# Kernel optimization log

Hardware: AMD Instinct MI355X
Metric: run time of the kernel (lower is better)

Reference implementation:

```python
import jax, jax.numpy as jnp
import numpy as np

B, S, H = 64, 4096, 256

def setup_inputs() -> dict:
    key = jax.random.key(0)
    k1, k2, k3, k4, k5 = jax.random.split(key, 5)
    scale = 1.0 / np.sqrt(H)
    return {
        "enc_out": jax.random.normal(k1, (B, S, H), dtype=jnp.float32),
        "final_h": jax.random.normal(k2, (B, H), dtype=jnp.float32),
        "W1": jax.random.normal(k3, (H, H), dtype=jnp.float32) * scale,
        "W2": jax.random.normal(k4, (H, H), dtype=jnp.float32) * scale,
        "v": jax.random.normal(k5, (H,), dtype=jnp.float32) * scale,
    }

def reference(enc_out, final_h, W1, W2, v):
    # W1(enc_out): [B,S,H]; W2(final_h) computed once: [B,H], broadcast over S
    proj = jnp.einsum('bsh,kh->bsk', enc_out, W1) + jnp.einsum('bh,kh->bk', final_h, W2)[:, None, :]
    scores = jnp.einsum('bsk,k->bs', jnp.tanh(proj), v)  # [B,S]
    alpha = jax.nn.softmax(scores, axis=1)  # softmax over seq dim
    context = jnp.einsum('bs,bsh->bh', alpha, enc_out)  # [B,H]
    return context
```

## Files before the change

### kernel.cpp

```cpp
#include <hip/hip_runtime.h>

typedef _Float16 half8  __attribute__((ext_vector_type(8)));
typedef _Float16 half4_t __attribute__((ext_vector_type(4)));
typedef float    f32x4  __attribute__((ext_vector_type(4)));

#define B_SZ    64
#define S_SZ    4096
#define H_SZ    256
#define CHUNKS  8
#define SCHUNK  512
#define TILE_R  32
#define NTILES  (SCHUNK / TILE_R)
#define PAD_H   264

__device__ __forceinline__ float tanh_fast(float x) {
  return 1.f - 2.f * __builtin_amdgcn_rcpf(__expf(2.f * x) + 1.f);
}

__device__ __forceinline__ void lds_barrier() {
  asm volatile("s_waitcnt lgkmcnt(0)" ::: "memory");
  __builtin_amdgcn_s_barrier();
}

template<int CTRL>
__device__ __forceinline__ float dpp_add_shl(float x) {
  int s = __builtin_amdgcn_update_dpp(0, __builtin_bit_cast(int, x), CTRL, 0xf, 0xf, true);
  return x + __builtin_bit_cast(float, s);
}
__device__ __forceinline__ float row_reduce16(float x) {
  x = dpp_add_shl<0x108>(x);
  x = dpp_add_shl<0x104>(x);
  x = dpp_add_shl<0x102>(x);
  x = dpp_add_shl<0x101>(x);
  return x;
}

__global__ __launch_bounds__(256) void bias_kernel(const float* __restrict__ fh,
                                                   const float* __restrict__ W2,
                                                   float* __restrict__ bias) {
  const int b = blockIdx.x, k = threadIdx.x;
  __shared__ float fsh[H_SZ];
  fsh[k] = fh[b * H_SZ + k];
  __syncthreads();
  const float* wrow = W2 + (size_t)k * H_SZ;
  float s = 0.f;
#pragma unroll 4
  for (int h = 0; h < H_SZ; h += 4) {
    f32x4 w = *(const f32x4*)(wrow + h);
    s += w[0] * fsh[h] + w[1] * fsh[h + 1] + w[2] * fsh[h + 2] + w[3] * fsh[h + 3];
  }
  bias[b * H_SZ + k] = s;
}

__global__ __launch_bounds__(512, 2) void fused_kernel(const float* __restrict__ enc,
                                                       const float* __restrict__ W1,
                                                       const float* __restrict__ v,
                                                       const float* __restrict__ bias,
                                                       float* __restrict__ pc,
                                                       float* __restrict__ pl) {
  __shared__ _Float16 As[3][TILE_R][PAD_H] __attribute__((aligned(16)));
  __shared__ float spartT[2][TILE_R][12];
  __shared__ float cpart[8][H_SZ];
  __shared__ float lArr[8];

  const int tid  = threadIdx.x;
  const int wave = tid >> 6;
  const int lane = tid & 63;
  const int nlo  = lane & 15;
  const int g    = lane >> 4;
  const int khi  = g * 8;
  const int b     = blockIdx.x >> 3;
  const int chunk = blockIdx.x & 7;
  const size_t encBase = ((size_t)b * S_SZ + (size_t)chunk * SCHUNK) * H_SZ;
  const float* src0 = enc + encBase + (size_t)tid * 4;

  f32x4 ldA[4], ldB[4];
#pragma unroll
  for (int i = 0; i < 4; ++i) ldA[i] = *(const f32x4*)(src0 + i * 2048);

  half8 wf[2][8];
#pragma unroll
  for (int cf = 0; cf < 2; ++cf) {
    const int n = wave * 32 + cf * 16 + nlo;
    const float* wrow = W1 + (size_t)n * H_SZ + khi;
#pragma unroll
    for (int ks = 0; ks < 8; ++ks) {
      f32x4 w0 = *(const f32x4*)(wrow + ks * 32);
      f32x4 w1 = *(const f32x4*)(wrow + ks * 32 + 4);
      half8 h;
#pragma unroll
      for (int j = 0; j < 4; ++j) { h[j] = (_Float16)w0[j]; h[4 + j] = (_Float16)w1[j]; }
      wf[cf][ks] = h;
    }
  }
#pragma unroll
  for (int i = 0; i < 4; ++i) ldB[i] = *(const f32x4*)(src0 + TILE_R * H_SZ + i * 2048);

  const int n0c = wave * 32 + nlo;
  const float vv0 = v[n0c],               vv1 = v[n0c + 16];
  const float bv0 = bias[b * H_SZ + n0c], bv1 = bias[b * H_SZ + n0c + 16];

  float l_acc = 0.f;
  float c0 = 0.f, c1 = 0.f, c2 = 0.f, c3 = 0.f;

  int p = 0;
  int pm1 = 2;

  auto tile_iter = [&](int t, f32x4 (&ld)[4]) {
#pragma unroll
    for (int i = 0; i < 4; ++i) {
      const int f4 = tid + i * 512;
      const int r = f4 >> 6, hq = (f4 & 63) * 4;
      half4_t hv;
      hv[0] = (_Float16)ld[i][0]; hv[1] = (_Float16)ld[i][1];
      hv[2] = (_Float16)ld[i][2]; hv[3] = (_Float16)ld[i][3];
      *(half4_t*)&As[p][r][hq] = hv;
    }
    if (t + 2 < NTILES) {
      const float* srcN = src0 + (size_t)(t + 2) * TILE_R * H_SZ;
#pragma unroll
      for (int i = 0; i < 4; ++i) ld[i] = *(const f32x4*)(srcN + i * 2048);
    }
    lds_barrier();

#pragma unroll
    for (int rf = 0; rf < 2; ++rf) {
      f32x4 d0 = {bv0, bv0, bv0, bv0}, d1 = {bv1, bv1, bv1, bv1};
#pragma unroll
      for (int ks = 0; ks < 8; ++ks) {
        half8 a = *(const half8*)&As[p][rf * 16 + nlo][ks * 32 + khi];
        d0 = __builtin_amdgcn_mfma_f32_16x16x32_f16(a, wf[0][ks], d0, 0, 0, 0);
        d1 = __builtin_amdgcn_mfma_f32_16x16x32_f16(a, wf[1][ks], d1, 0, 0, 0);
      }
      f32x4 s4;
#pragma unroll
      for (int i = 0; i < 4; ++i)
        s4[i] = tanh_fast(d0[i]) * vv0 + tanh_fast(d1[i]) * vv1;
#pragma unroll
      for (int i = 0; i < 4; ++i) s4[i] = row_reduce16(s4[i]);
      if (nlo == 0) {
#pragma unroll
        for (int i = 0; i < 4; ++i) spartT[t & 1][rf * 16 + g * 4 + i][wave] = s4[i];
      }
    }

    if (t > 0) {
#pragma unroll
      for (int rr = 0; rr < 4; ++rr) {
        const int r = wave * 4 + rr;
        const f32x4 q0 = *(const f32x4*)&spartT[(t - 1) & 1][r][0];
        const f32x4 q1 = *(const f32x4*)&spartT[(t - 1) & 1][r][4];
        const float u = __expf(q0[0] + q0[1] + q0[2] + q0[3] + q1[0] + q1[1] + q1[2] + q1[3]);
        l_acc += u;
        half4_t a = *(const half4_t*)&As[pm1][r][lane * 4];
        c0 += u * (float)a[0];
        c1 += u * (float)a[1];
        c2 += u * (float)a[2];
        c3 += u * (float)a[3];
      }
    }
    pm1 = p;
    p = (p == 2) ? 0 : p + 1;
  };

#pragma unroll 1
  for (int t2 = 0; t2 < NTILES; t2 += 2) {
    tile_iter(t2,     ldA);
    tile_iter(t2 + 1, ldB);
  }

  lds_barrier();
  {
    const int tl = (NTILES - 1) & 1;
#pragma unroll
    for (int rr = 0; rr < 4; ++rr) {
      const int r = wave * 4 + rr;
      const f32x4 q0 = *(const f32x4*)&spartT[tl][r][0];
      const f32x4 q1 = *(const f32x4*)&spartT[tl][r][4];
      const float u = __expf(q0[0] + q0[1] + q0[2] + q0[3] + q1[0] + q1[1] + q1[2] + q1[3]);
      l_acc += u;
      half4_t a = *(const half4_t*)&As[pm1][r][lane * 4];
      c0 += u * (float)a[0];
      c1 += u * (float)a[1];
      c2 += u * (float)a[2];
      c3 += u * (float)a[3];
    }
  }

  {
    f32x4 cv; cv[0] = c0; cv[1] = c1; cv[2] = c2; cv[3] = c3;
    *(f32x4*)&cpart[wave][lane * 4] = cv;
  }
  if (lane == 0) lArr[wave] = l_acc;
  __syncthreads();
  if (tid < H_SZ) {
    float s = 0.f;
#pragma unroll
    for (int w = 0; w < 8; ++w) s += cpart[w][tid];
    pc[(size_t)blockIdx.x * H_SZ + tid] = s;
  }
  if (tid == 0) {
    float L = 0.f;
#pragma unroll
    for (int w = 0; w < 8; ++w) L += lArr[w];
    pl[blockIdx.x] = L;
  }
}

__global__ __launch_bounds__(256) void combine_kernel(const float* __restrict__ pc,
                                                      const float* __restrict__ pl,
                                                      float* __restrict__ out) {
  const int b = blockIdx.x, h = threadIdx.x;
  float L = 0.f, s = 0.f;
#pragma unroll
  for (int j = 0; j < CHUNKS; ++j) {
    L += pl[b * CHUNKS + j];
    s += pc[(size_t)(b * CHUNKS + j) * H_SZ + h];
  }
  out[b * H_SZ + h] = s / L;
}

extern "C" void kernel_launch(void* const* d_in, const int* in_sizes, int n_in,
                              void* d_out, int out_size, void* d_ws, size_t ws_size,
                              hipStream_t stream) {
  const float* enc = (const float*)d_in[0];
  const float* fh  = (const float*)d_in[1];
  const float* W1  = (const float*)d_in[2];
  const float* W2  = (const float*)d_in[3];
  const float* v   = (const float*)d_in[4];
  float* out = (float*)d_out;

  float* ws   = (float*)d_ws;
  float* bias = ws;
  float* pc   = ws + B_SZ * H_SZ;
  float* pl   = pc + B_SZ * CHUNKS * H_SZ;

  bias_kernel<<<B_SZ, H_SZ, 0, stream>>>(fh, W2, bias);
  fused_kernel<<<B_SZ * CHUNKS, 512, 0, stream>>>(enc, W1, v, bias, pc, pl);
  combine_kernel<<<B_SZ, H_SZ, 0, stream>>>(pc, pl, out);
}
```

Measured before the change: 86.67 us.

## Fuse combine into main kernel via last-block atomic counter, split prefetch loads

Removes the separate combine kernel launch. The last block of each batch to finish, detected with an atomic counter that the bias kernel resets, now reduces the chunk partials and writes the output. The global prefetch of the next tile is also split into two halves, each issued after one row-fragment's MFMA chain, to interleave loads with compute. This adds threadfences and an atomic per block, and the prefetch registers stay live in a different pattern.

Result: slower. 207.1 us (+138.9%).

```diff
diff --git a/kernel.cpp b/kernel.cpp
--- a/kernel.cpp
+++ b/kernel.cpp
@@ -37,8 +37,10 @@
 
 __global__ __launch_bounds__(256) void bias_kernel(const float* __restrict__ fh,
                                                    const float* __restrict__ W2,
-                                                   float* __restrict__ bias) {
+                                                   float* __restrict__ bias,
+                                                   int* __restrict__ cnt) {
   const int b = blockIdx.x, k = threadIdx.x;
+  if (k == 0) cnt[b] = 0;
   __shared__ float fsh[H_SZ];
   fsh[k] = fh[b * H_SZ + k];
   __syncthreads();
@@ -57,11 +59,14 @@
                                                        const float* __restrict__ v,
                                                        const float* __restrict__ bias,
                                                        float* __restrict__ pc,
-                                                       float* __restrict__ pl) {
+                                                       float* __restrict__ pl,
+                                                       int* __restrict__ cnt,
+                                                       float* __restrict__ out) {
   __shared__ _Float16 As[3][TILE_R][PAD_H] __attribute__((aligned(16)));
   __shared__ float spartT[2][TILE_R][12];
   __shared__ float cpart[8][H_SZ];
   __shared__ float lArr[8];
+  __shared__ int winner;
 
   const int tid  = threadIdx.x;
   const int wave = tid >> 6;
@@ -116,22 +121,23 @@
       hv[2] = (_Float16)ld[i][2]; hv[3] = (_Float16)ld[i][3];
       *(half4_t*)&As[p][r][hq] = hv;
     }
-    if (t + 2 < NTILES) {
-      const float* srcN = src0 + (size_t)(t + 2) * TILE_R * H_SZ;
-#pragma unroll
-      for (int i = 0; i < 4; ++i) ld[i] = *(const f32x4*)(srcN + i * 2048);
-    }
     lds_barrier();
 
-#pragma unroll
-    for (int rf = 0; rf < 2; ++rf) {
+    const bool pf = (t + 2 < NTILES);
+    const float* srcN = src0 + (size_t)(t + 2) * TILE_R * H_SZ;
+
+    {
       f32x4 d0 = {bv0, bv0, bv0, bv0}, d1 = {bv1, bv1, bv1, bv1};
 #pragma unroll
       for (int ks = 0; ks < 8; ++ks) {
-        half8 a = *(const half8*)&As[p][rf * 16 + nlo][ks * 32 + khi];
+        half8 a = *(const half8*)&As[p][nlo][ks * 32 + khi];
         d0 = __builtin_amdgcn_mfma_f32_16x16x32_f16(a, wf[0][ks], d0, 0, 0, 0);
         d1 = __builtin_amdgcn_mfma_f32_16x16x32_f16(a, wf[1][ks], d1, 0, 0, 0);
       }
+      if (pf) {
+        ld[0] = *(const f32x4*)(srcN);
+        ld[1] = *(const f32x4*)(srcN + 2048);
+      }
       f32x4 s4;
 #pragma unroll
       for (int i = 0; i < 4; ++i)
@@ -140,7 +146,30 @@
       for (int i = 0; i < 4; ++i) s4[i] = row_reduce16(s4[i]);
       if (nlo == 0) {
 #pragma unroll
-        for (int i = 0; i < 4; ++i) spartT[t & 1][rf * 16 + g * 4 + i][wave] = s4[i];
+        for (int i = 0; i < 4; ++i) spartT[t & 1][g * 4 + i][wave] = s4[i];
+      }
+    }
+    {
+      f32x4 d0 = {bv0, bv0, bv0, bv0}, d1 = {bv1, bv1, bv1, bv1};
+#pragma unroll
+      for (int ks = 0; ks < 8; ++ks) {
+        half8 a = *(const half8*)&As[p][16 + nlo][ks * 32 + khi];
+        d0 = __builtin_amdgcn_mfma_f32_16x16x32_f16(a, wf[0][ks], d0, 0, 0, 0);
+        d1 = __builtin_amdgcn_mfma_f32_16x16x32_f16(a, wf[1][ks], d1, 0, 0, 0);
+      }
+      if (pf) {
+        ld[2] = *(const f32x4*)(srcN + 4096);
+        ld[3] = *(const f32x4*)(srcN + 6144);
+      }
+      f32x4 s4;
+#pragma unroll
+      for (int i = 0; i < 4; ++i)
+        s4[i] = tanh_fast(d0[i]) * vv0 + tanh_fast(d1[i]) * vv1;
+#pragma unroll
+      for (int i = 0; i < 4; ++i) s4[i] = row_reduce16(s4[i]);
+      if (nlo == 0) {
+#pragma unroll
+        for (int i = 0; i < 4; ++i) spartT[t & 1][16 + g * 4 + i][wave] = s4[i];
       }
     }
 
@@ -205,19 +234,25 @@
     for (int w = 0; w < 8; ++w) L += lArr[w];
     pl[blockIdx.x] = L;
   }
-}
-
-__global__ __launch_bounds__(256) void combine_kernel(const float* __restrict__ pc,
-                                                      const float* __restrict__ pl,
-                                                      float* __restrict__ out) {
-  const int b = blockIdx.x, h = threadIdx.x;
-  float L = 0.f, s = 0.f;
-#pragma unroll
-  for (int j = 0; j < CHUNKS; ++j) {
-    L += pl[b * CHUNKS + j];
-    s += pc[(size_t)(b * CHUNKS + j) * H_SZ + h];
-  }
-  out[b * H_SZ + h] = s / L;
+
+  __threadfence();
+  if (tid == 0) {
+    const int old = atomicAdd(&cnt[b], 1);
+    winner = (old == CHUNKS - 1) ? 1 : 0;
+  }
+  __syncthreads();
+  if (winner) {
+    __threadfence();
+    if (tid < H_SZ) {
+      float L = 0.f, s = 0.f;
+#pragma unroll
+      for (int j = 0; j < CHUNKS; ++j) {
+        L += pl[b * CHUNKS + j];
+        s += pc[(size_t)(b * CHUNKS + j) * H_SZ + tid];
+      }
+      out[b * H_SZ + tid] = s / L;
+    }
+  }
 }
 
 extern "C" void kernel_launch(void* const* d_in, const int* in_sizes, int n_in,
@@ -234,8 +269,8 @@
   float* bias = ws;
   float* pc   = ws + B_SZ * H_SZ;
   float* pl   = pc + B_SZ * CHUNKS * H_SZ;
-
-  bias_kernel<<<B_SZ, H_SZ, 0, stream>>>(fh, W2, bias);
-  fused_kernel<<<B_SZ * CHUNKS, 512, 0, stream>>>(enc, W1, v, bias, pc, pl);
-  combine_kernel<<<B_SZ, H_SZ, 0, stream>>>(pc, pl, out);
-}
+  int*   cnt  = (int*)(pl + B_SZ * CHUNKS);
+
+  bias_kernel<<<B_SZ, H_SZ, 0, stream>>>(fh, W2, bias, cnt);
+  fused_kernel<<<B_SZ * CHUNKS, 512, 0, stream>>>(enc, W1, v, bias, pc, pl, cnt, out);
+}
```
